# Optimization experiments

Hardware: AMD Instinct MI355X
Metric: run time of the kernel (lower is better)

## Reference

```python
import jax, jax.numpy as jnp
import numpy as np

N = 50000
E = 800000
IN_CH = 256
OUT_CH = 64   # per-head channels (PyG out_channels)
HEADS = 4
NEG_SLOPE = 0.2


def setup_inputs() -> dict:
    key = jax.random.key(0)
    k = jax.random.split(key, 8)
    x = jax.random.normal(k[0], (N, IN_CH), dtype=jnp.float32)
    edge_index = jax.random.randint(k[1], (2, E), 0, N, dtype=jnp.int64)
    # GATConv parameters
    W = jax.random.normal(k[2], (IN_CH, HEADS * OUT_CH), dtype=jnp.float32) * (1.0 / np.sqrt(IN_CH))
    att_src = jax.random.normal(k[3], (HEADS, OUT_CH), dtype=jnp.float32) * 0.1
    att_dst = jax.random.normal(k[4], (HEADS, OUT_CH), dtype=jnp.float32) * 0.1
    bias = jnp.zeros((OUT_CH,), dtype=jnp.float32)
    # residual linear (bias=False)
    W_res = jax.random.normal(k[5], (IN_CH, OUT_CH), dtype=jnp.float32) * (1.0 / np.sqrt(IN_CH))
    return {"x": x, "edge_index": edge_index, "W": W, "att_src": att_src,
            "att_dst": att_dst, "bias": bias, "W_res": W_res}


def _gat_forward(x, edge_index, W, att_src, att_dst, bias, W_res):
    # residual branch
    x_res = x @ W_res                                   # [N, OUT_CH]

    # node transform: [N, H, C]
    xw = (x @ W).reshape(N, HEADS, OUT_CH)
    # per-node attention logits, [N, H]
    a_src = jnp.einsum('nhc,hc->nh', xw, att_src)
    a_dst = jnp.einsum('nhc,hc->nh', xw, att_dst)

    # add self-loops (PyG GATConv default add_self_loops=True)
    loops = jnp.arange(N, dtype=edge_index.dtype)
    src = jnp.concatenate([edge_index[0], loops])       # [E+N]
    dst = jnp.concatenate([edge_index[1], loops])       # [E+N]

    # per-edge logits + leaky relu, [E+N, H]
    alpha = jax.nn.leaky_relu(a_src[src] + a_dst[dst], NEG_SLOPE)

    # segment softmax over destination nodes
    m = jax.ops.segment_max(alpha, dst, num_segments=N)    # [N, H]
    e = jnp.exp(alpha - m[dst])
    denom = jax.ops.segment_sum(e, dst, num_segments=N)    # [N, H]
    a = e / denom[dst]                                     # [E+N, H]
    # (dropout p=0.1 on attention coeffs is identity in eval mode)

    # weighted scatter-aggregate: [N, H, C]
    msgs = xw[src] * a[:, :, None]
    out = jax.ops.segment_sum(msgs, dst, num_segments=N)

    # concat=False -> mean over heads, then bias
    x_conv = out.mean(axis=1) + bias                     # [N, OUT_CH]
    return jax.nn.relu(x_conv + x_res)


def reference(x, edge_index, W, att_src, att_dst, bias, W_res):
    return _gat_forward(x, edge_index, W, att_src, att_dst, bias, W_res)
```

## Files before the change

kernel.cpp:

```cpp
#include <hip/hip_runtime.h>
#include <math.h>

#define N_NODES 50000
#define N_EDGES 800000
#define IN_CH   256
#define OUT_CH  64
#define HEADS   4
#define NEG_SLOPE 0.2f
#define NCOLS   320
#define NTILES  20
#define NKK     8
#define PACK_BLOCKS 40
#define GEMM_BLOCKS 782
#define SCAN_BLOCKS 196
#define HIST_BLOCKS 3125
#define SCAT_BLOCKS 3125
#define LOGIT_BLOCKS 12500

typedef __attribute__((ext_vector_type(8))) short short8;
typedef __attribute__((ext_vector_type(4))) float f32x4;

__device__ __forceinline__ float lrelu(float v) {
    return v > 0.f ? v : NEG_SLOPE * v;
}
__device__ __forceinline__ unsigned bf16_rne(float f) {
    unsigned u = __float_as_uint(f);
    return (u + 0x7FFFu + ((u >> 16) & 1u)) >> 16;
}
__device__ __forceinline__ unsigned pack2(float lo, float hi) {
    return bf16_rne(lo) | (bf16_rne(hi) << 16);
}
__device__ __forceinline__ float bflo(unsigned u) { return __uint_as_float(u << 16); }
__device__ __forceinline__ float bfhi(unsigned u) { return __uint_as_float(u & 0xFFFF0000u); }
__device__ __forceinline__ short8 as_short8(uint4 u) {
    union { uint4 u4; short8 s8; } cv; cv.u4 = u; return cv.s8;
}

__global__ __launch_bounds__(256) void pack_B(
    const float* __restrict__ W, const float* __restrict__ Wres,
    uint4* __restrict__ Bp)
{
    const int idx  = blockIdx.x * 256 + threadIdx.x;
    const int kk   = idx / (NTILES * 64);
    const int rem  = idx - kk * (NTILES * 64);
    const int t    = rem >> 6;
    const int lane = rem & 63;
    const int colL = lane & 15, quad = lane >> 4;
    const int col  = t * 16 + colL;
    const int k0   = kk * 32 + quad * 8;
    float v[8];
    #pragma unroll
    for (int j = 0; j < 8; ++j) {
        const int k = k0 + j;
        v[j] = (col < IN_CH) ? W[(size_t)k * IN_CH + col]
                             : Wres[(size_t)k * OUT_CH + (col - IN_CH)];
    }
    uint4 u;
    u.x = pack2(v[0], v[1]); u.y = pack2(v[2], v[3]);
    u.z = pack2(v[4], v[5]); u.w = pack2(v[6], v[7]);
    Bp[(kk * NTILES + t) * 64 + lane] = u;
}

__global__ __launch_bounds__(256) void hist_gemm(
    const float* __restrict__ x, const uint4* __restrict__ Bp,
    uint2* __restrict__ xw2, float* __restrict__ xres,
    const int* __restrict__ ei, int* __restrict__ cnt,
    int* __restrict__ epos)
{
    __shared__ uint4 Alds[4 * NKK * 64];

    if (blockIdx.x >= GEMM_BLOCKS) {
        const int e = (blockIdx.x - GEMM_BLOCKS) * 256 + threadIdx.x;
        if (e < N_EDGES)
            epos[e] = atomicAdd(&cnt[ei[N_EDGES + e]], 1);
        return;
    }

    const int tid = threadIdx.x;
    const int n0  = blockIdx.x * 64;

    #pragma unroll
    for (int i = 0; i < 8; ++i) {
        const int e    = i * 256 + tid;
        const int g    = e >> 9;
        const int kk   = (e >> 6) & 7;
        const int lane = e & 63;
        const int cL   = lane & 15, qd = lane >> 4;
        const int row  = n0 + g * 16 + cL;
        const int k0   = kk * 32 + qd * 8;
        uint4 u = make_uint4(0u, 0u, 0u, 0u);
        if (row < N_NODES) {
            const float4 a = *reinterpret_cast<const float4*>(x + (size_t)row * IN_CH + k0);
            const float4 b = *reinterpret_cast<const float4*>(x + (size_t)row * IN_CH + k0 + 4);
            u.x = pack2(a.x, a.y); u.y = pack2(a.z, a.w);
            u.z = pack2(b.x, b.y); u.w = pack2(b.z, b.w);
        }
        Alds[(g * NKK + kk) * 64 + lane] = u;
    }
    __syncthreads();

    const int lane = tid & 63;
    const int wv   = tid >> 6;
    const int colL = lane & 15, quad = lane >> 4;

    f32x4 acc[4][5];
    #pragma unroll
    for (int rg = 0; rg < 4; ++rg)
        #pragma unroll
        for (int j = 0; j < 5; ++j) acc[rg][j] = (f32x4){0.f, 0.f, 0.f, 0.f};

    for (int kk = 0; kk < NKK; ++kk) {
        uint4 bu[5];
        #pragma unroll
        for (int j = 0; j < 5; ++j)
            bu[j] = Bp[(kk * NTILES + j * 4 + wv) * 64 + lane];
        #pragma unroll
        for (int rg = 0; rg < 4; ++rg) {
            const short8 a = as_short8(Alds[(rg * NKK + kk) * 64 + lane]);
            #pragma unroll
            for (int j = 0; j < 5; ++j)
                acc[rg][j] = __builtin_amdgcn_mfma_f32_16x16x32_bf16(
                    a, as_short8(bu[j]), acc[rg][j], 0, 0, 0);
        }
    }

    #pragma unroll
    for (int rg = 0; rg < 4; ++rg) {
        #pragma unroll
        for (int r = 0; r < 4; ++r) {
            const int row = n0 + rg * 16 + quad * 4 + r;
            if (row < N_NODES) {
                xw2[(size_t)row * 64 + wv * 16 + colL] = make_uint2(
                    pack2(acc[rg][0][r], acc[rg][1][r]),
                    pack2(acc[rg][2][r], acc[rg][3][r]));
                xres[(size_t)row * OUT_CH + wv * 16 + colL] = acc[rg][4][r];
            }
        }
    }
}

__global__ __launch_bounds__(256) void scan_local(
    const int* __restrict__ cnt, int* __restrict__ lscan, int* __restrict__ bsum)
{
    __shared__ int ws[4];
    const int t = threadIdx.x, lane = t & 63, w = t >> 6;
    const int i = blockIdx.x * 256 + t;
    const int v = (i < N_NODES) ? cnt[i] : 0;
    int sc = v;
    #pragma unroll
    for (int off = 1; off < 64; off <<= 1) {
        const int n = __shfl_up(sc, off);
        if (lane >= off) sc += n;
    }
    if (lane == 63) ws[w] = sc;
    __syncthreads();
    int prefix = 0;
    for (int j = 0; j < w; ++j) prefix += ws[j];
    if (i < N_NODES) lscan[i] = prefix + sc - v;
    if (t == 255) bsum[blockIdx.x] = prefix + sc;
}

__global__ __launch_bounds__(256) void scatter_logits(
    const int* __restrict__ ei, const int* __restrict__ epos,
    const int* __restrict__ lscan, const int* __restrict__ bsum,
    int* __restrict__ esrc,
    const uint2* __restrict__ xw2, const float* __restrict__ attS,
    const float* __restrict__ attD, float* __restrict__ asrc,
    float* __restrict__ adst)
{
    const int t = threadIdx.x;
    const int lane = t & 63, wv = t >> 6;

    if (blockIdx.x < SCAT_BLOCKS) {
        __shared__ int bsx[256];
        __shared__ int ws[4];
        const int v = (t < SCAN_BLOCKS) ? bsum[t] : 0;
        int sc = v;
        #pragma unroll
        for (int off = 1; off < 64; off <<= 1) {
            const int n = __shfl_up(sc, off);
            if (lane >= off) sc += n;
        }
        if (lane == 63) ws[wv] = sc;
        __syncthreads();
        int prefix = 0;
        for (int j = 0; j < wv; ++j) prefix += ws[j];
        bsx[t] = prefix + sc - v;
        __syncthreads();

        const int e = blockIdx.x * 256 + t;
        if (e < N_EDGES) {
            const int d = ei[N_EDGES + e];
            esrc[lscan[d] + bsx[d >> 8] + epos[e]] = ei[e];
        }
        return;
    }

    const int n = (blockIdx.x - SCAT_BLOCKS) * 4 + wv;
    const uint2 v = xw2[(size_t)n * 64 + lane];
    const float h0 = bflo(v.x), h1 = bfhi(v.x), h2 = bflo(v.y), h3 = bfhi(v.y);
    float s0 = h0 * attS[lane],       s1 = h1 * attS[64 + lane];
    float s2 = h2 * attS[128 + lane], s3 = h3 * attS[192 + lane];
    float d0 = h0 * attD[lane],       d1 = h1 * attD[64 + lane];
    float d2 = h2 * attD[128 + lane], d3 = h3 * attD[192 + lane];
    #pragma unroll
    for (int off = 32; off >= 1; off >>= 1) {
        s0 += __shfl_xor(s0, off); s1 += __shfl_xor(s1, off);
        s2 += __shfl_xor(s2, off); s3 += __shfl_xor(s3, off);
        d0 += __shfl_xor(d0, off); d1 += __shfl_xor(d1, off);
        d2 += __shfl_xor(d2, off); d3 += __shfl_xor(d3, off);
    }
    if (lane == 0)
        *reinterpret_cast<float4*>(asrc + (size_t)n * 4) = make_float4(s0, s1, s2, s3);
    if (lane == 1)
        *reinterpret_cast<float4*>(adst + (size_t)n * 4) = make_float4(d0, d1, d2, d3);
}

__global__ __launch_bounds__(256) void aggregate(
    const int* __restrict__ esrc, const int* __restrict__ lscan,
    const int* __restrict__ bsum, const int* __restrict__ cnt,
    const float* __restrict__ asrc, const float* __restrict__ adst,
    const uint2* __restrict__ xw2, const float* __restrict__ xres,
    const float* __restrict__ bias, float* __restrict__ out)
{
    __shared__ float4 wbuf[4][64];
    __shared__ int    sbuf[4][64];
    __shared__ int    bsx[256];
    __shared__ int    ws[4];
    const int t = threadIdx.x;
    const int lane = t & 63;
    const int wv   = t >> 6;

    {
        const int v = (t < SCAN_BLOCKS) ? bsum[t] : 0;
        int sc = v;
        #pragma unroll
        for (int off = 1; off < 64; off <<= 1) {
            const int n = __shfl_up(sc, off);
            if (lane >= off) sc += n;
        }
        if (lane == 63) ws[wv] = sc;
        __syncthreads();
        int prefix = 0;
        for (int j = 0; j < wv; ++j) prefix += ws[j];
        bsx[t] = prefix + sc - v;
        __syncthreads();
    }

    const int d = blockIdx.x * 4 + wv;
    const int row = lscan[d] + bsx[d >> 8];
    const int deg = cnt[d];
    const float4 ad = *reinterpret_cast<const float4*>(adst + (size_t)d * 4);
    const char* xwB = (const char*)xw2;
    const int laneB = lane << 3;

    float dn0 = 0.f, dn1 = 0.f, dn2 = 0.f, dn3 = 0.f;
    float ac0 = 0.f, ac1 = 0.f, ac2 = 0.f, ac3 = 0.f;

    for (int base = 0; base < deg; base += 64) {
        const int m = min(64, deg - base);
        if (lane < m) {
            const int s = esrc[row + base + lane];
            const float4 as = *reinterpret_cast<const float4*>(asrc + (size_t)s * 4);
            const float e0 = __expf(lrelu(as.x + ad.x));
            const float e1 = __expf(lrelu(as.y + ad.y));
            const float e2 = __expf(lrelu(as.z + ad.z));
            const float e3 = __expf(lrelu(as.w + ad.w));
            dn0 += e0; dn1 += e1; dn2 += e2; dn3 += e3;
            wbuf[wv][lane] = make_float4(e0, e1, e2, e3);
            sbuf[wv][lane] = s << 9;
        }
        int j = 0;
        for (; j + 4 <= m; j += 4) {
            uint2 v0 = *(const uint2*)(xwB + sbuf[wv][j]     + laneB);
            uint2 v1 = *(const uint2*)(xwB + sbuf[wv][j + 1] + laneB);
            uint2 v2 = *(const uint2*)(xwB + sbuf[wv][j + 2] + laneB);
            uint2 v3 = *(const uint2*)(xwB + sbuf[wv][j + 3] + laneB);
            {
                const float4 w = wbuf[wv][j];
                ac0 = fmaf(w.x, bflo(v0.x), ac0); ac1 = fmaf(w.y, bfhi(v0.x), ac1);
                ac2 = fmaf(w.z, bflo(v0.y), ac2); ac3 = fmaf(w.w, bfhi(v0.y), ac3);
            }
            {
                const float4 w = wbuf[wv][j + 1];
                ac0 = fmaf(w.x, bflo(v1.x), ac0); ac1 = fmaf(w.y, bfhi(v1.x), ac1);
                ac2 = fmaf(w.z, bflo(v1.y), ac2); ac3 = fmaf(w.w, bfhi(v1.y), ac3);
            }
            {
                const float4 w = wbuf[wv][j + 2];
                ac0 = fmaf(w.x, bflo(v2.x), ac0); ac1 = fmaf(w.y, bfhi(v2.x), ac1);
                ac2 = fmaf(w.z, bflo(v2.y), ac2); ac3 = fmaf(w.w, bfhi(v2.y), ac3);
            }
            {
                const float4 w = wbuf[wv][j + 3];
                ac0 = fmaf(w.x, bflo(v3.x), ac0); ac1 = fmaf(w.y, bfhi(v3.x), ac1);
                ac2 = fmaf(w.z, bflo(v3.y), ac2); ac3 = fmaf(w.w, bfhi(v3.y), ac3);
            }
        }
        for (; j < m; ++j) {
            const float4 w = wbuf[wv][j];
            const uint2 v = *(const uint2*)(xwB + sbuf[wv][j] + laneB);
            ac0 = fmaf(w.x, bflo(v.x), ac0);
            ac1 = fmaf(w.y, bfhi(v.x), ac1);
            ac2 = fmaf(w.z, bflo(v.y), ac2);
            ac3 = fmaf(w.w, bfhi(v.y), ac3);
        }
    }

    #pragma unroll
    for (int off = 32; off >= 1; off >>= 1) {
        dn0 += __shfl_xor(dn0, off);
        dn1 += __shfl_xor(dn1, off);
        dn2 += __shfl_xor(dn2, off);
        dn3 += __shfl_xor(dn3, off);
    }
    const float4 asd = *reinterpret_cast<const float4*>(asrc + (size_t)d * 4);
    const float s0 = __expf(lrelu(asd.x + ad.x));
    const float s1 = __expf(lrelu(asd.y + ad.y));
    const float s2 = __expf(lrelu(asd.z + ad.z));
    const float s3 = __expf(lrelu(asd.w + ad.w));
    const uint2 u = xw2[(size_t)d * 64 + lane];
    ac0 = fmaf(s0, bflo(u.x), ac0); ac1 = fmaf(s1, bfhi(u.x), ac1);
    ac2 = fmaf(s2, bflo(u.y), ac2); ac3 = fmaf(s3, bfhi(u.y), ac3);
    const float i0 = 0.25f / (dn0 + s0);
    const float i1 = 0.25f / (dn1 + s1);
    const float i2 = 0.25f / (dn2 + s2);
    const float i3 = 0.25f / (dn3 + s3);
    const float v = ac0 * i0 + ac1 * i1 + ac2 * i2 + ac3 * i3
                  + bias[lane] + xres[(size_t)d * OUT_CH + lane];
    out[(size_t)d * OUT_CH + lane] = fmaxf(v, 0.f);
}

extern "C" void kernel_launch(void* const* d_in, const int* in_sizes, int n_in,
                              void* d_out, int out_size, void* d_ws, size_t ws_size,
                              hipStream_t stream) {
    const float* x    = (const float*)d_in[0];
    const int*   ei   = (const int*)d_in[1];
    const float* W    = (const float*)d_in[2];
    const float* attS = (const float*)d_in[3];
    const float* attD = (const float*)d_in[4];
    const float* bias = (const float*)d_in[5];
    const float* Wres = (const float*)d_in[6];
    float* out = (float*)d_out;

    char* p = (char*)d_ws;
    uint4*    Bp    = (uint4*)p;    p += (size_t)NKK * NTILES * 64 * 16;
    uint2*    xw2   = (uint2*)p;    p += (size_t)N_NODES * 64 * 8;
    float*    xres  = (float*)p;    p += (size_t)N_NODES * OUT_CH * 4;
    float*    asrc  = (float*)p;    p += (size_t)N_NODES * HEADS * 4;
    float*    adst  = (float*)p;    p += (size_t)N_NODES * HEADS * 4;
    int*      cnt   = (int*)p;      p += (size_t)N_NODES * 4;
    int*      lscan = (int*)p;      p += (size_t)N_NODES * 4;
    int*      bsum  = (int*)p;      p += 256 * 4;
    int*      epos  = (int*)p;      p += (size_t)N_EDGES * 4;
    int*      esrc  = (int*)p;      p += (size_t)N_EDGES * 4;

    hipMemsetAsync(cnt, 0, (size_t)N_NODES * sizeof(int), stream);

    pack_B<<<PACK_BLOCKS, 256, 0, stream>>>(W, Wres, Bp);
    hist_gemm<<<GEMM_BLOCKS + HIST_BLOCKS, 256, 0, stream>>>(
        x, Bp, xw2, xres, ei, cnt, epos);
    scan_local<<<SCAN_BLOCKS, 256, 0, stream>>>(cnt, lscan, bsum);
    scatter_logits<<<SCAT_BLOCKS + LOGIT_BLOCKS, 256, 0, stream>>>(
        ei, epos, lscan, bsum, esrc, xw2, attS, attD, asrc, adst);
    aggregate<<<LOGIT_BLOCKS, 256, 0, stream>>>(
        esrc, lscan, bsum, cnt, asrc, adst, xw2, xres, bias, out);
}
```

Measured before the change: 245.5 us.

## Fuse attention logit computation into GEMM epilogue and split aggregate launch

Computes per-node source/destination attention logits inside the GEMM epilogue from the fp32 accumulators, using shuffle reductions and shared-memory atomics. This removes the separate logit blocks that re-read xw from global memory. The aggregate kernel is also split into two launches over node halves via an offset parameter. The costs are extra epilogue work and LDS atomics in the GEMM, plus one more launch. Logits are now taken from fp32 accumulators rather than bf16-rounded values, so numerics shift slightly.

```diff
diff --git a/kernel.cpp b/kernel.cpp
--- a/kernel.cpp
+++ b/kernel.cpp
@@ -15,7 +15,7 @@
 #define SCAN_BLOCKS 196
 #define HIST_BLOCKS 3125
 #define SCAT_BLOCKS 3125
-#define LOGIT_BLOCKS 12500
+#define AGG_BLOCKS  6250
 
 typedef __attribute__((ext_vector_type(8))) short short8;
 typedef __attribute__((ext_vector_type(4))) float f32x4;
@@ -65,9 +65,13 @@
     const float* __restrict__ x, const uint4* __restrict__ Bp,
     uint2* __restrict__ xw2, float* __restrict__ xres,
     const int* __restrict__ ei, int* __restrict__ cnt,
-    int* __restrict__ epos)
+    int* __restrict__ epos,
+    const float* __restrict__ attS, const float* __restrict__ attD,
+    float* __restrict__ asrc, float* __restrict__ adst)
 {
     __shared__ uint4 Alds[4 * NKK * 64];
+    __shared__ float logS[64][HEADS];
+    __shared__ float logD[64][HEADS];
 
     if (blockIdx.x >= GEMM_BLOCKS) {
         const int e = (blockIdx.x - GEMM_BLOCKS) * 256 + threadIdx.x;
@@ -78,6 +82,9 @@
 
     const int tid = threadIdx.x;
     const int n0  = blockIdx.x * 64;
+
+    logS[tid >> 2][tid & 3] = 0.f;
+    logD[tid >> 2][tid & 3] = 0.f;
 
     #pragma unroll
     for (int i = 0; i < 8; ++i) {
@@ -137,6 +144,42 @@
             }
         }
     }
+
+    float aSr[HEADS], aDr[HEADS];
+    #pragma unroll
+    for (int h = 0; h < HEADS; ++h) {
+        aSr[h] = attS[h * 64 + wv * 16 + colL];
+        aDr[h] = attD[h * 64 + wv * 16 + colL];
+    }
+    #pragma unroll
+    for (int rg = 0; rg < 4; ++rg) {
+        #pragma unroll
+        for (int h = 0; h < HEADS; ++h) {
+            #pragma unroll
+            for (int r = 0; r < 4; ++r) {
+                float vS = acc[rg][h][r] * aSr[h];
+                float vD = acc[rg][h][r] * aDr[h];
+                #pragma unroll
+                for (int m = 1; m < 16; m <<= 1) {
+                    vS += __shfl_xor(vS, m);
+                    vD += __shfl_xor(vD, m);
+                }
+                if (colL == 0) {
+                    atomicAdd(&logS[rg * 16 + quad * 4 + r][h], vS);
+                    atomicAdd(&logD[rg * 16 + quad * 4 + r][h], vD);
+                }
+            }
+        }
+    }
+    __syncthreads();
+    {
+        const int rl = tid >> 2, h = tid & 3;
+        const int row = n0 + rl;
+        if (row < N_NODES) {
+            asrc[(size_t)row * HEADS + h] = logS[rl][h];
+            adst[(size_t)row * HEADS + h] = logD[rl][h];
+        }
+    }
 }
 
 __global__ __launch_bounds__(256) void scan_local(
@@ -160,60 +203,35 @@
     if (t == 255) bsum[blockIdx.x] = prefix + sc;
 }
 
-__global__ __launch_bounds__(256) void scatter_logits(
+__global__ __launch_bounds__(256) void scatter_edges(
     const int* __restrict__ ei, const int* __restrict__ epos,
     const int* __restrict__ lscan, const int* __restrict__ bsum,
-    int* __restrict__ esrc,
-    const uint2* __restrict__ xw2, const float* __restrict__ attS,
-    const float* __restrict__ attD, float* __restrict__ asrc,
-    float* __restrict__ adst)
-{
+    int* __restrict__ esrc)
+{
+    __shared__ int bsx[256];
+    __shared__ int ws[4];
     const int t = threadIdx.x;
     const int lane = t & 63, wv = t >> 6;
 
-    if (blockIdx.x < SCAT_BLOCKS) {
-        __shared__ int bsx[256];
-        __shared__ int ws[4];
-        const int v = (t < SCAN_BLOCKS) ? bsum[t] : 0;
-        int sc = v;
-        #pragma unroll
-        for (int off = 1; off < 64; off <<= 1) {
-            const int n = __shfl_up(sc, off);
-            if (lane >= off) sc += n;
-        }
-        if (lane == 63) ws[wv] = sc;
-        __syncthreads();
-        int prefix = 0;
-        for (int j = 0; j < wv; ++j) prefix += ws[j];
-        bsx[t] = prefix + sc - v;
-        __syncthreads();
-
-        const int e = blockIdx.x * 256 + t;
-        if (e < N_EDGES) {
-            const int d = ei[N_EDGES + e];
-            esrc[lscan[d] + bsx[d >> 8] + epos[e]] = ei[e];
-        }
-        return;
-    }
-
-    const int n = (blockIdx.x - SCAT_BLOCKS) * 4 + wv;
-    const uint2 v = xw2[(size_t)n * 64 + lane];
-    const float h0 = bflo(v.x), h1 = bfhi(v.x), h2 = bflo(v.y), h3 = bfhi(v.y);
-    float s0 = h0 * attS[lane],       s1 = h1 * attS[64 + lane];
-    float s2 = h2 * attS[128 + lane], s3 = h3 * attS[192 + lane];
-    float d0 = h0 * attD[lane],       d1 = h1 * attD[64 + lane];
-    float d2 = h2 * attD[128 + lane], d3 = h3 * attD[192 + lane];
-    #pragma unroll
-    for (int off = 32; off >= 1; off >>= 1) {
-        s0 += __shfl_xor(s0, off); s1 += __shfl_xor(s1, off);
-        s2 += __shfl_xor(s2, off); s3 += __shfl_xor(s3, off);
-        d0 += __shfl_xor(d0, off); d1 += __shfl_xor(d1, off);
-        d2 += __shfl_xor(d2, off); d3 += __shfl_xor(d3, off);
-    }
-    if (lane == 0)
-        *reinterpret_cast<float4*>(asrc + (size_t)n * 4) = make_float4(s0, s1, s2, s3);
-    if (lane == 1)
-        *reinterpret_cast<float4*>(adst + (size_t)n * 4) = make_float4(d0, d1, d2, d3);
+    const int v = (t < SCAN_BLOCKS) ? bsum[t] : 0;
+    int sc = v;
+    #pragma unroll
+    for (int off = 1; off < 64; off <<= 1) {
+        const int n = __shfl_up(sc, off);
+        if (lane >= off) sc += n;
+    }
+    if (lane == 63) ws[wv] = sc;
+    __syncthreads();
+    int prefix = 0;
+    for (int j = 0; j < wv; ++j) prefix += ws[j];
+    bsx[t] = prefix + sc - v;
+    __syncthreads();
+
+    const int e = blockIdx.x * 256 + t;
+    if (e < N_EDGES) {
+        const int d = ei[N_EDGES + e];
+        esrc[lscan[d] + bsx[d >> 8] + epos[e]] = ei[e];
+    }
 }
 
 __global__ __launch_bounds__(256) void aggregate(
@@ -221,7 +239,8 @@
     const int* __restrict__ bsum, const int* __restrict__ cnt,
     const float* __restrict__ asrc, const float* __restrict__ adst,
     const uint2* __restrict__ xw2, const float* __restrict__ xres,
-    const float* __restrict__ bias, float* __restrict__ out)
+    const float* __restrict__ bias, float* __restrict__ out,
+    const int d0)
 {
     __shared__ float4 wbuf[4][64];
     __shared__ int    sbuf[4][64];
@@ -247,7 +266,7 @@
         __syncthreads();
     }
 
-    const int d = blockIdx.x * 4 + wv;
+    const int d = d0 + blockIdx.x * 4 + wv;
     const int row = lscan[d] + bsx[d >> 8];
     const int deg = cnt[d];
     const float4 ad = *reinterpret_cast<const float4*>(adst + (size_t)d * 4);
@@ -359,10 +378,12 @@
 
     pack_B<<<PACK_BLOCKS, 256, 0, stream>>>(W, Wres, Bp);
     hist_gemm<<<GEMM_BLOCKS + HIST_BLOCKS, 256, 0, stream>>>(
-        x, Bp, xw2, xres, ei, cnt, epos);
+        x, Bp, xw2, xres, ei, cnt, epos, attS, attD, asrc, adst);
     scan_local<<<SCAN_BLOCKS, 256, 0, stream>>>(cnt, lscan, bsum);
-    scatter_logits<<<SCAT_BLOCKS + LOGIT_BLOCKS, 256, 0, stream>>>(
-        ei, epos, lscan, bsum, esrc, xw2, attS, attD, asrc, adst);
-    aggregate<<<LOGIT_BLOCKS, 256, 0, stream>>>(
-        esrc, lscan, bsum, cnt, asrc, adst, xw2, xres, bias, out);
-}
+    scatter_edges<<<SCAT_BLOCKS, 256, 0, stream>>>(
+        ei, epos, lscan, bsum, esrc);
+    aggregate<<<AGG_BLOCKS, 256, 0, stream>>>(
+        esrc, lscan, bsum, cnt, asrc, adst, xw2, xres, bias, out, 0);
+    aggregate<<<AGG_BLOCKS, 256, 0, stream>>>(
+        esrc, lscan, bsum, cnt, asrc, adst, xw2, xres, bias, out, 25000);
+}
```

Result: slower. 253.3 us (+3.2%).
